# Kernel tuning notes

Hardware: AMD Instinct MI355X
Metric: run time of the kernel (lower is better)

The kernel has to match this reference:

```python
import jax, jax.numpy as jnp
import numpy as np


def setup_inputs() -> dict:
    key = jax.random.key(0)
    k1, k2 = jax.random.split(key)
    B, H, W, D, C = 4, 128, 128, 128, 2
    image = jax.random.normal(k1, (B, H, W, D, C), dtype=jnp.float32)
    # near-identity affine so sampling is meaningful (localization-net output stand-in)
    theta = 0.1 * jax.random.normal(k2, (B, 3, 4), dtype=jnp.float32) + jnp.eye(3, 4, dtype=jnp.float32)[None]
    return {"image": image, "theta": theta}


def reference(image, theta):
    # Faithful port of SpatialTransformer._transform / _interpolate (incl. its
    # original index-flattening and z-weight (z1 - z0) conventions).
    B, H, W, D, C = image.shape
    oH, oW, oD = H, W, D  # downsample_factor = 1
    N = oH * oW * oD

    # _meshgrid: tf.meshgrid default 'xy' indexing -> shapes (oH, oW, oD)
    xl = jnp.linspace(-1.0, 1.0, oW)
    yl = jnp.linspace(-1.0, 1.0, oH)
    zl = jnp.linspace(-1.0, 1.0, oD)
    Xg, Yg, Zg = jnp.meshgrid(xl, yl, zl)
    grid = jnp.stack([Xg.ravel(), Yg.ravel(), Zg.ravel(), jnp.ones(N, jnp.float32)], 0)  # [4, N]

    tg = jnp.einsum('bij,jn->bin', theta.astype(jnp.float32), grid)  # [B, 3, N]
    x = tg[:, 0, :].reshape(-1)
    y = tg[:, 1, :].reshape(-1)
    z = tg[:, 2, :].reshape(-1)

    # map from [-1, 1] to pixel coords (original uses full extent, not extent-1)
    x = 0.5 * (x + 1.0) * W
    y = 0.5 * (y + 1.0) * H
    z = 0.5 * (z + 1.0) * D

    x0 = jnp.floor(x).astype(jnp.int32); x1 = x0 + 1
    y0 = jnp.floor(y).astype(jnp.int32); y1 = y0 + 1
    z0 = jnp.floor(z).astype(jnp.int32); z1 = z0 + 1
    x0 = jnp.clip(x0, 0, W - 1); x1 = jnp.clip(x1, 0, W - 1)
    y0 = jnp.clip(y0, 0, H - 1); y1 = jnp.clip(y1, 0, H - 1)
    z0 = jnp.clip(z0, 0, D - 1); z1 = jnp.clip(z1, 0, D - 1)

    base = jnp.repeat(jnp.arange(B, dtype=jnp.int32) * (H * W * D), N)  # [B*N]
    # original flat-index convention: base + y*W + z*W*H + x
    b00 = base + y0 * W + z0 * (W * H)
    b10 = base + y1 * W + z0 * (W * H)
    b01 = base + y0 * W + z1 * (W * H)
    b11 = base + y1 * W + z1 * (W * H)

    flat = image.reshape(-1, C).astype(jnp.float32)  # [B*H*W*D, C]
    pa = flat[b00 + x0]; pb = flat[b10 + x0]
    pc = flat[b00 + x1]; pd = flat[b10 + x1]
    pe = flat[b01 + x0]; pf = flat[b11 + x0]
    pg = flat[b01 + x1]; ph = flat[b11 + x1]

    x0f = x0.astype(jnp.float32); x1f = x1.astype(jnp.float32)
    y0f = y0.astype(jnp.float32); y1f = y1.astype(jnp.float32)
    z0f = z0.astype(jnp.float32); z1f = z1.astype(jnp.float32)

    wa = ((x1f - x) * (y1f - y) * (z1f - z))[:, None]
    wb = ((x1f - x) * (y - y0f) * (z1f - z))[:, None]
    wc = ((x - x0f) * (y1f - y) * (z1f - z))[:, None]
    wd = ((x - x0f) * (y - y0f) * (z1f - z))[:, None]
    we = ((x1f - x) * (y1f - y) * (z1f - z0f))[:, None]
    wf = ((x1f - x) * (y - y0f) * (z1f - z0f))[:, None]
    wg = ((x - x0f) * (y1f - y) * (z1f - z0f))[:, None]
    wh = ((x - x0f) * (y - y0f) * (z1f - z0f))[:, None]

    out = (wa * pa + wb * pb + wc * pc + wd * pd
           + we * pe + wf * pf + wg * pg + wh * ph)  # [B*N, C]
    return out.reshape(B, oH, oW, oD, C)
```

## Files before the change

kernel.cpp:

```cpp
#include <hip/hip_runtime.h>
#include <math.h>

#define BN 4
#define HN 128
#define WN 128
#define DN 128

__global__ __launch_bounds__(128) void st_trilerp_kernel(
    const float* __restrict__ image,
    const float* __restrict__ theta,
    float* __restrict__ out)
{
    const int bi = blockIdx.z;
    const int b  = bi >> 7;
    const int i  = bi & (HN - 1);
    const int j0 = blockIdx.y << 4;
    const int k0 = blockIdx.x << 4;

    const int tid = threadIdx.x;
    const int jj  = tid & 15;
    const int ktg = tid >> 4;
    const int j   = j0 + jj;
    const int kb  = k0 + (ktg << 1);

    const double step = 2.0 / 127.0;
    const double X = (j == WN - 1) ? 1.0 : (double)j * step - 1.0;
    const double Y = (i == HN - 1) ? 1.0 : (double)i * step - 1.0;

    const float* th = theta + b * 12;
    const double t0 = (double)th[0], t1 = (double)th[1], t2  = (double)th[2],  t3  = (double)th[3];
    const double t4 = (double)th[4], t5 = (double)th[5], t6  = (double)th[6],  t7  = (double)th[7];
    const double t8 = (double)th[8], t9 = (double)th[9], t10 = (double)th[10], t11 = (double)th[11];

    const double KST = 128.0 / 127.0;
    const double Px = t2  * KST, Qx = fma(64.0, (t0*X + t1*Y) + t3  - t2,  64.0);
    const double Py = t6  * KST, Qy = fma(64.0, (t4*X + t5*Y) + t7  - t6,  64.0);
    const double Pz = t10 * KST, Qz = fma(64.0, (t8*X + t9*Y) + t11 - t10, 64.0);

    const int base = b * (HN * WN * DN);
    const float2* __restrict__ img2 = (const float2*)image;

    float4 q00[2], q10[2], q01[2], q11[2];
    float  wxL[2], wxH[2], wy0[2], wy1[2], wz0[2], wzA[2];

#pragma unroll
    for (int c = 0; c < 2; ++c) {
        const double kd = (double)(kb + c);
        const double x = fma(Px, kd, Qx);
        const double y = fma(Py, kd, Qy);
        const double z = fma(Pz, kd, Qz);

        const double xf = floor(x), yf = floor(y), zf = floor(z);
        const int x0u = (int)xf, y0u = (int)yf, z0u = (int)zf;
        const int x0 = min(max(x0u,     0), WN - 1);
        const int x1 = min(max(x0u + 1, 0), WN - 1);
        const int y0 = min(max(y0u,     0), HN - 1);
        const int y1 = min(max(y0u + 1, 0), HN - 1);
        const int z0 = min(max(z0u,     0), DN - 1);
        const int z1 = min(max(z0u + 1, 0), DN - 1);

        const float xs = (float)x, ys = (float)y, zs = (float)z;
        const float wx0f = (float)x1 - xs, wx1f = xs - (float)x0;
        wy0[c] = (float)y1 - ys;  wy1[c] = ys - (float)y0;
        wz0[c] = (float)z1 - zs;  wzA[c] = (float)(z1 - z0);

        const int xb  = min(x0, WN - 2);
        const bool lo0 = (x0 == xb), lo1 = (x1 == xb);
        wxL[c] = (lo0 ? wx0f : 0.0f) + (lo1 ? wx1f : 0.0f);
        wxH[c] = (lo0 ? 0.0f : wx0f) + (lo1 ? 0.0f : wx1f);

        const int r00 = base + (y0 << 7) + (z0 << 14) + xb;
        const int dy  = (y1 - y0) << 7;
        const int dz  = (z1 - z0) << 14;
        q00[c] = *(const float4*)(img2 + r00);
        q10[c] = *(const float4*)(img2 + r00 + dy);
        q01[c] = *(const float4*)(img2 + r00 + dz);
        q11[c] = *(const float4*)(img2 + r00 + dy + dz);
    }

    float ox[2], oy[2];
#pragma unroll
    for (int c = 0; c < 2; ++c) {
        const float g00x = wxL[c]*q00[c].x + wxH[c]*q00[c].z;
        const float g00y = wxL[c]*q00[c].y + wxH[c]*q00[c].w;
        const float g10x = wxL[c]*q10[c].x + wxH[c]*q10[c].z;
        const float g10y = wxL[c]*q10[c].y + wxH[c]*q10[c].w;
        const float g01x = wxL[c]*q01[c].x + wxH[c]*q01[c].z;
        const float g01y = wxL[c]*q01[c].y + wxH[c]*q01[c].w;
        const float g11x = wxL[c]*q11[c].x + wxH[c]*q11[c].z;
        const float g11y = wxL[c]*q11[c].y + wxH[c]*q11[c].w;

        const float h0x = wy0[c]*g00x + wy1[c]*g10x;
        const float h0y = wy0[c]*g00y + wy1[c]*g10y;
        const float h1x = wy0[c]*g01x + wy1[c]*g11x;
        const float h1y = wy0[c]*g01y + wy1[c]*g11y;

        ox[c] = wz0[c]*h0x + wzA[c]*h1x;
        oy[c] = wz0[c]*h0y + wzA[c]*h1y;
    }

    const int oidx = (bi * WN + j) * DN + kb;
    *(float4*)((float2*)out + oidx) = make_float4(ox[0], oy[0], ox[1], oy[1]);
}

extern "C" void kernel_launch(void* const* d_in, const int* in_sizes, int n_in,
                              void* d_out, int out_size, void* d_ws, size_t ws_size,
                              hipStream_t stream) {
    const float* image = (const float*)d_in[0];
    const float* theta = (const float*)d_in[1];
    float* out = (float*)d_out;

    dim3 grid(DN / 16, WN / 16, BN * HN);
    st_trilerp_kernel<<<grid, 128, 0, stream>>>(image, theta, out);
}
```

Before: 150.7 us.

## Raise per-thread samples to four, stage outputs via LDS for coalesced stores

Each thread now computes four depth samples instead of two, with the tile covering 32 columns by 16 depths. Gathers use inline-asm dwordx4 loads, and staged vmcnt waits let each sample be combined as soon as its loads arrive. Results go through a padded shared-memory tile and are rewritten so consecutive threads store contiguous depth chunks. This aims to raise memory-level parallelism and improve store coalescing, at the cost of more registers, an LDS barrier, and manual waitcnt handling that bypasses compiler scheduling.

Measured after the change: 151.5 us. Within noise of the previous version (+0.6%).

```diff
diff --git a/kernel.cpp b/kernel.cpp
--- a/kernel.cpp
+++ b/kernel.cpp
@@ -5,6 +5,13 @@
 #define HN 128
 #define WN 128
 #define DN 128
+
+
+#define GLOAD16(dst, ptr) \
+    asm volatile("global_load_dwordx4 %0, %1, off" : "=v"(dst) : "v"(ptr))
+#define VMWAIT(n) do { \
+    asm volatile("s_waitcnt vmcnt(" #n ")" ::: "memory"); \
+    __builtin_amdgcn_sched_barrier(0); } while (0)
 
 __global__ __launch_bounds__(128) void st_trilerp_kernel(
     const float* __restrict__ image,
@@ -14,14 +21,14 @@
     const int bi = blockIdx.z;
     const int b  = bi >> 7;
     const int i  = bi & (HN - 1);
-    const int j0 = blockIdx.y << 4;
+    const int j0 = blockIdx.y << 5;
     const int k0 = blockIdx.x << 4;
 
     const int tid = threadIdx.x;
-    const int jj  = tid & 15;
-    const int ktg = tid >> 4;
+    const int jj  = tid & 31;
+    const int kg  = tid >> 5;
     const int j   = j0 + jj;
-    const int kb  = k0 + (ktg << 1);
+    const int kb  = k0 + (kg << 2);
 
     const double step = 2.0 / 127.0;
     const double X = (j == WN - 1) ? 1.0 : (double)j * step - 1.0;
@@ -40,11 +47,11 @@
     const int base = b * (HN * WN * DN);
     const float2* __restrict__ img2 = (const float2*)image;
 
-    float4 q00[2], q10[2], q01[2], q11[2];
-    float  wxL[2], wxH[2], wy0[2], wy1[2], wz0[2], wzA[2];
+    float4 q00[4], q10[4], q01[4], q11[4];
+    float  wxL[4], wxH[4], wy0[4], wy1[4], wz0[4], wzA[4];
 
 #pragma unroll
-    for (int c = 0; c < 2; ++c) {
+    for (int c = 0; c < 4; ++c) {
         const double kd = (double)(kb + c);
         const double x = fma(Px, kd, Qx);
         const double y = fma(Py, kd, Qy);
@@ -69,38 +76,53 @@
         wxL[c] = (lo0 ? wx0f : 0.0f) + (lo1 ? wx1f : 0.0f);
         wxH[c] = (lo0 ? 0.0f : wx0f) + (lo1 ? 0.0f : wx1f);
 
-        const int r00 = base + (y0 << 7) + (z0 << 14) + xb;
-        const int dy  = (y1 - y0) << 7;
-        const int dz  = (z1 - z0) << 14;
-        q00[c] = *(const float4*)(img2 + r00);
-        q10[c] = *(const float4*)(img2 + r00 + dy);
-        q01[c] = *(const float4*)(img2 + r00 + dz);
-        q11[c] = *(const float4*)(img2 + r00 + dy + dz);
+        const int rb = base + (y0 << 7) + (z0 << 14) + xb;
+        const int dy = (y1 - y0) << 7;
+        const int dz = (z1 - z0) << 14;
+        GLOAD16(q00[c], img2 + rb);
+        GLOAD16(q10[c], img2 + rb + dy);
+        GLOAD16(q01[c], img2 + rb + dz);
+        GLOAD16(q11[c], img2 + rb + dy + dz);
     }
 
-    float ox[2], oy[2];
+    __shared__ float2 tile[16][33];
+    const int kk = kg << 2;
+
+#define COMBINE(c) do { \
+        const float g00x = wxL[c]*q00[c].x + wxH[c]*q00[c].z; \
+        const float g00y = wxL[c]*q00[c].y + wxH[c]*q00[c].w; \
+        const float g10x = wxL[c]*q10[c].x + wxH[c]*q10[c].z; \
+        const float g10y = wxL[c]*q10[c].y + wxH[c]*q10[c].w; \
+        const float g01x = wxL[c]*q01[c].x + wxH[c]*q01[c].z; \
+        const float g01y = wxL[c]*q01[c].y + wxH[c]*q01[c].w; \
+        const float g11x = wxL[c]*q11[c].x + wxH[c]*q11[c].z; \
+        const float g11y = wxL[c]*q11[c].y + wxH[c]*q11[c].w; \
+        const float h0x = wy0[c]*g00x + wy1[c]*g10x; \
+        const float h0y = wy0[c]*g00y + wy1[c]*g10y; \
+        const float h1x = wy0[c]*g01x + wy1[c]*g11x; \
+        const float h1y = wy0[c]*g01y + wy1[c]*g11y; \
+        tile[kk + c][jj] = make_float2(wz0[c]*h0x + wzA[c]*h1x, \
+                                       wz0[c]*h0y + wzA[c]*h1y); \
+    } while (0)
+
+    VMWAIT(12); COMBINE(0);
+    VMWAIT(8);  COMBINE(1);
+    VMWAIT(4);  COMBINE(2);
+    VMWAIT(0);  COMBINE(3);
+#undef COMBINE
+
+    __syncthreads();
+
+    const int row = tid >> 2;
+    const int c0  = tid & 3;
 #pragma unroll
-    for (int c = 0; c < 2; ++c) {
-        const float g00x = wxL[c]*q00[c].x + wxH[c]*q00[c].z;
-        const float g00y = wxL[c]*q00[c].y + wxH[c]*q00[c].w;
-        const float g10x = wxL[c]*q10[c].x + wxH[c]*q10[c].z;
-        const float g10y = wxL[c]*q10[c].y + wxH[c]*q10[c].w;
-        const float g01x = wxL[c]*q01[c].x + wxH[c]*q01[c].z;
-        const float g01y = wxL[c]*q01[c].y + wxH[c]*q01[c].w;
-        const float g11x = wxL[c]*q11[c].x + wxH[c]*q11[c].z;
-        const float g11y = wxL[c]*q11[c].y + wxH[c]*q11[c].w;
-
-        const float h0x = wy0[c]*g00x + wy1[c]*g10x;
-        const float h0y = wy0[c]*g00y + wy1[c]*g10y;
-        const float h1x = wy0[c]*g01x + wy1[c]*g11x;
-        const float h1y = wy0[c]*g01y + wy1[c]*g11y;
-
-        ox[c] = wz0[c]*h0x + wzA[c]*h1x;
-        oy[c] = wz0[c]*h0y + wzA[c]*h1y;
+    for (int s = 0; s < 2; ++s) {
+        const int col = c0 + (s << 2);
+        const float2 a = tile[2*col + 0][row];
+        const float2 d = tile[2*col + 1][row];
+        const int oidx = (bi * WN + (j0 + row)) * DN + k0 + 2*col;
+        *(float4*)((float2*)out + oidx) = make_float4(a.x, a.y, d.x, d.y);
     }
-
-    const int oidx = (bi * WN + j) * DN + kb;
-    *(float4*)((float2*)out + oidx) = make_float4(ox[0], oy[0], ox[1], oy[1]);
 }
 
 extern "C" void kernel_launch(void* const* d_in, const int* in_sizes, int n_in,
@@ -110,6 +132,6 @@
     const float* theta = (const float*)d_in[1];
     float* out = (float*)d_out;
 
-    dim3 grid(DN / 16, WN / 16, BN * HN);
+    dim3 grid(DN / 16, WN / 32, BN * HN);
     st_trilerp_kernel<<<grid, 128, 0, stream>>>(image, theta, out);
 }
```

## Software-pipeline gathers across eight k-tiles per thread with XCD-aware block remap

Applied to the files above, without the earlier changes.

Launches 2048 blocks of 256 threads instead of many small 128-thread blocks. Each thread now walks eight depth tiles, computing the next tile's weights and addresses while the current tile's gathers are in flight. Gathers are issued through inline-asm dwordx4 loads with explicit vmcnt waits. The block index is swizzled so neighbouring work lands on the same XCD for L2 locality, and output is written with nontemporal stores. In exchange, each batch waits on vmcnt(0), so only one batch of loads is in flight per thread. The fewer, larger blocks may also give less wave-level parallelism to hide gather latency.

Result: slower. 189.8 us (+26.0%).

```diff
diff --git a/kernel.cpp b/kernel.cpp
--- a/kernel.cpp
+++ b/kernel.cpp
@@ -6,22 +6,35 @@
 #define WN 128
 #define DN 128
 
-__global__ __launch_bounds__(128) void st_trilerp_kernel(
+
+typedef float f32x4 __attribute__((ext_vector_type(4)));
+
+#define GLOAD16(dst, ptr) \
+    asm volatile("global_load_dwordx4 %0, %1, off" \
+                 : "=&v"(dst) : "v"(ptr) : "memory")
+#define VMWAIT0() do { \
+    __builtin_amdgcn_sched_barrier(0); \
+    asm volatile("s_waitcnt vmcnt(0)" ::: "memory"); \
+    __builtin_amdgcn_sched_barrier(0); } while (0)
+
+__global__ __launch_bounds__(256, 1) void st_trilerp_kernel(
     const float* __restrict__ image,
     const float* __restrict__ theta,
     float* __restrict__ out)
 {
-    const int bi = blockIdx.z;
+    const int orig = blockIdx.x;
+    const int wgid = ((orig & 7) << 8) | (orig >> 3);
+    const int bi = wgid >> 2;
+    const int jt = wgid & 3;
     const int b  = bi >> 7;
     const int i  = bi & (HN - 1);
-    const int j0 = blockIdx.y << 4;
-    const int k0 = blockIdx.x << 4;
+    const int j0 = jt << 5;
 
     const int tid = threadIdx.x;
-    const int jj  = tid & 15;
-    const int ktg = tid >> 4;
+    const int jj  = tid & 31;
+    const int kg  = tid >> 5;
     const int j   = j0 + jj;
-    const int kb  = k0 + (ktg << 1);
+    const int kbth = kg << 1;
 
     const double step = 2.0 / 127.0;
     const double X = (j == WN - 1) ? 1.0 : (double)j * step - 1.0;
@@ -39,68 +52,99 @@
 
     const int base = b * (HN * WN * DN);
     const float2* __restrict__ img2 = (const float2*)image;
+    const int orow = (bi * WN + j) * DN + kbth;
 
-    float4 q00[2], q10[2], q01[2], q11[2];
-    float  wxL[2], wxH[2], wy0[2], wy1[2], wz0[2], wzA[2];
+    float4 qa0, qa1, qb0, qb1, qc0, qc1, qd0, qd1;
+    int    rA0, rA1, rB0, rB1, rC0, rC1, rD0, rD1;
+    float  wxLA0, wxLA1, wxLB0, wxLB1, wxHA0, wxHA1, wxHB0, wxHB1;
+    float  wy0A0, wy0A1, wy0B0, wy0B1, wy1A0, wy1A1, wy1B0, wy1B1;
+    float  wz0A0, wz0A1, wz0B0, wz0B1, wzAA0, wzAA1, wzAB0, wzAB1;
 
-#pragma unroll
-    for (int c = 0; c < 2; ++c) {
-        const double kd = (double)(kb + c);
-        const double x = fma(Px, kd, Qx);
-        const double y = fma(Py, kd, Qy);
-        const double z = fma(Pz, kd, Qz);
+#define AW1(WS, T, C) do { \
+    const double kd = (double)(((T) << 4) + kbth + (C)); \
+    const double x = fma(Px, kd, Qx); \
+    const double y = fma(Py, kd, Qy); \
+    const double z = fma(Pz, kd, Qz); \
+    const double xf = floor(x), yf = floor(y), zf = floor(z); \
+    const int x0u = (int)xf, y0u = (int)yf, z0u = (int)zf; \
+    const int x0 = min(max(x0u,     0), WN - 1); \
+    const int x1 = min(max(x0u + 1, 0), WN - 1); \
+    const int y0 = min(max(y0u,     0), HN - 1); \
+    const int y1 = min(max(y0u + 1, 0), HN - 1); \
+    const int z0 = min(max(z0u,     0), DN - 1); \
+    const int z1 = min(max(z0u + 1, 0), DN - 1); \
+    const float xs = (float)x, ys = (float)y, zs = (float)z; \
+    const float wx0f = (float)x1 - xs, wx1f = xs - (float)x0; \
+    wy0##WS##C = (float)y1 - ys;  wy1##WS##C = ys - (float)y0; \
+    wz0##WS##C = (float)z1 - zs;  wzA##WS##C = (float)(z1 - z0); \
+    const int xb  = min(x0, WN - 2); \
+    const bool lo0 = (x0 == xb), lo1 = (x1 == xb); \
+    wxL##WS##C = (lo0 ? wx0f : 0.0f) + (lo1 ? wx1f : 0.0f); \
+    wxH##WS##C = (lo0 ? 0.0f : wx0f) + (lo1 ? 0.0f : wx1f); \
+    const int rb = base + (y0 << 7) + (z0 << 14) + xb; \
+    const int dy = (y1 - y0) << 7; \
+    const int dz = (z1 - z0) << 14; \
+    rA##C = rb;      rB##C = rb + dy; \
+    rC##C = rb + dz; rD##C = rb + dy + dz; \
+} while (0)
 
-        const double xf = floor(x), yf = floor(y), zf = floor(z);
-        const int x0u = (int)xf, y0u = (int)yf, z0u = (int)zf;
-        const int x0 = min(max(x0u,     0), WN - 1);
-        const int x1 = min(max(x0u + 1, 0), WN - 1);
-        const int y0 = min(max(y0u,     0), HN - 1);
-        const int y1 = min(max(y0u + 1, 0), HN - 1);
-        const int z0 = min(max(z0u,     0), DN - 1);
-        const int z1 = min(max(z0u + 1, 0), DN - 1);
+#define AW(WS, T) do { AW1(WS, T, 0); AW1(WS, T, 1); } while (0)
 
-        const float xs = (float)x, ys = (float)y, zs = (float)z;
-        const float wx0f = (float)x1 - xs, wx1f = xs - (float)x0;
-        wy0[c] = (float)y1 - ys;  wy1[c] = ys - (float)y0;
-        wz0[c] = (float)z1 - zs;  wzA[c] = (float)(z1 - z0);
+#define ISSUE() do { \
+    GLOAD16(qa0, img2 + rA0); \
+    GLOAD16(qb0, img2 + rB0); \
+    GLOAD16(qc0, img2 + rC0); \
+    GLOAD16(qd0, img2 + rD0); \
+    GLOAD16(qa1, img2 + rA1); \
+    GLOAD16(qb1, img2 + rB1); \
+    GLOAD16(qc1, img2 + rC1); \
+    GLOAD16(qd1, img2 + rD1); \
+} while (0)
 
-        const int xb  = min(x0, WN - 2);
-        const bool lo0 = (x0 == xb), lo1 = (x1 == xb);
-        wxL[c] = (lo0 ? wx0f : 0.0f) + (lo1 ? wx1f : 0.0f);
-        wxH[c] = (lo0 ? 0.0f : wx0f) + (lo1 ? 0.0f : wx1f);
+#define COMB1(WS, C) do { \
+    const float gax = wxL##WS##C*qa##C.x + wxH##WS##C*qa##C.z; \
+    const float gay = wxL##WS##C*qa##C.y + wxH##WS##C*qa##C.w; \
+    const float gbx = wxL##WS##C*qb##C.x + wxH##WS##C*qb##C.z; \
+    const float gby = wxL##WS##C*qb##C.y + wxH##WS##C*qb##C.w; \
+    const float gcx = wxL##WS##C*qc##C.x + wxH##WS##C*qc##C.z; \
+    const float gcy = wxL##WS##C*qc##C.y + wxH##WS##C*qc##C.w; \
+    const float gdx = wxL##WS##C*qd##C.x + wxH##WS##C*qd##C.z; \
+    const float gdy = wxL##WS##C*qd##C.y + wxH##WS##C*qd##C.w; \
+    const float h0x = wy0##WS##C*gax + wy1##WS##C*gbx; \
+    const float h0y = wy0##WS##C*gay + wy1##WS##C*gby; \
+    const float h1x = wy0##WS##C*gcx + wy1##WS##C*gdx; \
+    const float h1y = wy0##WS##C*gcy + wy1##WS##C*gdy; \
+    ox##C = wz0##WS##C*h0x + wzA##WS##C*h1x; \
+    oy##C = wz0##WS##C*h0y + wzA##WS##C*h1y; \
+} while (0)
 
-        const int r00 = base + (y0 << 7) + (z0 << 14) + xb;
-        const int dy  = (y1 - y0) << 7;
-        const int dz  = (z1 - z0) << 14;
-        q00[c] = *(const float4*)(img2 + r00);
-        q10[c] = *(const float4*)(img2 + r00 + dy);
-        q01[c] = *(const float4*)(img2 + r00 + dz);
-        q11[c] = *(const float4*)(img2 + r00 + dy + dz);
-    }
+#define TAIL(WS, T, DO_ISSUE) do { \
+    float ox0, oy0, ox1, oy1; \
+    COMB1(WS, 0); \
+    COMB1(WS, 1); \
+    if (DO_ISSUE) { ISSUE(); } \
+    f32x4 val; val.x = ox0; val.y = oy0; val.z = ox1; val.w = oy1; \
+    __builtin_nontemporal_store(val, \
+        (f32x4*)((float2*)out + orow + ((T) << 4))); \
+} while (0)
 
-    float ox[2], oy[2];
-#pragma unroll
-    for (int c = 0; c < 2; ++c) {
-        const float g00x = wxL[c]*q00[c].x + wxH[c]*q00[c].z;
-        const float g00y = wxL[c]*q00[c].y + wxH[c]*q00[c].w;
-        const float g10x = wxL[c]*q10[c].x + wxH[c]*q10[c].z;
-        const float g10y = wxL[c]*q10[c].y + wxH[c]*q10[c].w;
-        const float g01x = wxL[c]*q01[c].x + wxH[c]*q01[c].z;
-        const float g01y = wxL[c]*q01[c].y + wxH[c]*q01[c].w;
-        const float g11x = wxL[c]*q11[c].x + wxH[c]*q11[c].z;
-        const float g11y = wxL[c]*q11[c].y + wxH[c]*q11[c].w;
+    AW(A, 0);
+    ISSUE();
 
-        const float h0x = wy0[c]*g00x + wy1[c]*g10x;
-        const float h0y = wy0[c]*g00y + wy1[c]*g10y;
-        const float h1x = wy0[c]*g01x + wy1[c]*g11x;
-        const float h1y = wy0[c]*g01y + wy1[c]*g11y;
+    AW(B, 1); VMWAIT0(); TAIL(A, 0, 1);
+    AW(A, 2); VMWAIT0(); TAIL(B, 1, 1);
+    AW(B, 3); VMWAIT0(); TAIL(A, 2, 1);
+    AW(A, 4); VMWAIT0(); TAIL(B, 3, 1);
+    AW(B, 5); VMWAIT0(); TAIL(A, 4, 1);
+    AW(A, 6); VMWAIT0(); TAIL(B, 5, 1);
+    AW(B, 7); VMWAIT0(); TAIL(A, 6, 1);
+    VMWAIT0(); TAIL(B, 7, 0);
 
-        ox[c] = wz0[c]*h0x + wzA[c]*h1x;
-        oy[c] = wz0[c]*h0y + wzA[c]*h1y;
-    }
-
-    const int oidx = (bi * WN + j) * DN + kb;
-    *(float4*)((float2*)out + oidx) = make_float4(ox[0], oy[0], ox[1], oy[1]);
+#undef TAIL
+#undef COMB1
+#undef ISSUE
+#undef AW
+#undef AW1
 }
 
 extern "C" void kernel_launch(void* const* d_in, const int* in_sizes, int n_in,
@@ -110,6 +154,5 @@
     const float* theta = (const float*)d_in[1];
     float* out = (float*)d_out;
 
-    dim3 grid(DN / 16, WN / 16, BN * HN);
-    st_trilerp_kernel<<<grid, 128, 0, stream>>>(image, theta, out);
+    st_trilerp_kernel<<<dim3(2048), 256, 0, stream>>>(image, theta, out);
 }
```
